# Kernel optimization log

Hardware: AMD Instinct MI355X
Metric: run time of the kernel (lower is better)

The kernel has to match this reference:

```python
import jax, jax.numpy as jnp
import numpy as np
import math

N_HEADS = 16
D_MODEL = 1024
DK = D_MODEL // N_HEADS
B, S = 2, 2048


def setup_inputs() -> dict:
    key = jax.random.key(0)
    ks = jax.random.split(key, 11)
    scale_in = 1.0 / math.sqrt(D_MODEL)
    scale_o = 1.0 / math.sqrt(N_HEADS * DK)
    return {
        "query": jax.random.normal(ks[0], (B, S, D_MODEL), jnp.float32),
        "key": jax.random.normal(ks[1], (B, S, D_MODEL), jnp.float32),
        "value": jax.random.normal(ks[2], (B, S, D_MODEL), jnp.float32),
        # stacked per-head projection weights [H, d_model, dk], biases [H, dk]
        "Wq": jax.random.normal(ks[3], (N_HEADS, D_MODEL, DK), jnp.float32) * scale_in,
        "bq": jax.random.normal(ks[4], (N_HEADS, DK), jnp.float32) * scale_in,
        "Wk": jax.random.normal(ks[5], (N_HEADS, D_MODEL, DK), jnp.float32) * scale_in,
        "bk": jax.random.normal(ks[6], (N_HEADS, DK), jnp.float32) * scale_in,
        "Wv": jax.random.normal(ks[7], (N_HEADS, D_MODEL, DK), jnp.float32) * scale_in,
        "bv": jax.random.normal(ks[8], (N_HEADS, DK), jnp.float32) * scale_in,
        "Wo": jax.random.normal(ks[9], (N_HEADS * DK, D_MODEL), jnp.float32) * scale_o,
        "bo": jax.random.normal(ks[10], (D_MODEL,), jnp.float32) * scale_o,
    }


def reference(query, key, value, Wq, bq, Wk, bk, Wv, bv, Wo, bo):
    # Per-head linear projections, vectorized over heads: [B,H,S,dk]
    q = jnp.einsum("bsd,hdk->bhsk", query, Wq) + bq[None, :, None, :]
    k = jnp.einsum("bsd,hdk->bhsk", key, Wk) + bk[None, :, None, :]
    v = jnp.einsum("bsd,hdk->bhsk", value, Wv) + bv[None, :, None, :]
    # Scaled dot-product scores [B,H,S,S]
    scores = jnp.einsum("bhsk,bhtk->bhst", q, k) / jnp.sqrt(jnp.asarray(DK, q.dtype))
    # FAITHFUL to source: nn.Softmax(dim=0) -> softmax over the BATCH axis
    attn = jax.nn.softmax(scores, axis=0)
    out = jnp.einsum("bhst,bhtk->bhsk", attn, v)  # [B,H,S,dk]
    # concat heads along feature dim (torch.cat dim=2)
    concat = out.transpose(0, 2, 1, 3).reshape(query.shape[0], query.shape[1], N_HEADS * DK)
    return concat @ Wo + bo
```

## Files before the change

kernel.cpp:

```cpp
#include <hip/hip_runtime.h>
#include <hip/hip_bf16.h>

#define B_ 2
#define S_ 2048
#define D_ 1024
#define H_ 16
#define DK_ 64
#define BS_ (B_ * S_)

typedef unsigned int u32;
typedef unsigned short u16;
typedef __attribute__((ext_vector_type(8))) short bf16x8;
typedef __attribute__((ext_vector_type(4))) float f32x4;

__device__ __forceinline__ float bf2f(u16 v) {
    union { u32 u; float f; } c; c.u = ((u32)v) << 16; return c.f;
}
__device__ __forceinline__ u16 f2bf(float f) {
    union { float f; u32 u; } c; c.f = f;
    u32 u = c.u;
    return (u16)((u + 0x7fffu + ((u >> 16) & 1u)) >> 16);
}
__device__ __forceinline__ u32 packtr(float lo, float hi) {
    union { float f; u32 u; } a, b; a.f = lo; b.f = hi;
    return __builtin_amdgcn_perm(b.u, a.u, 0x07060302u);
}
__device__ __forceinline__ int sw64(int r, int c8) { return (((c8) + (r)) & 7) * 8; }

struct WArgs { const float* W[4]; u16* WT[4]; float* csums; };
__global__ __launch_bounds__(256) void prep_w(WArgs wa)
{
    __shared__ __attribute__((aligned(16))) u16 T[64][72];
    const int z = blockIdx.z;
    const float* W = wa.W[z];
    u16* WT = wa.WT[z];
    const int headMode = (z < 3) ? 1 : 0;
    const int tid = threadIdx.x;
    if (z == 0 && blockIdx.x == 0 && blockIdx.y == 0) {
        float4 zz = {0.f, 0.f, 0.f, 0.f};
        *(float4*)(wa.csums + tid * 4) = zz;
    }
    const int k0 = blockIdx.x * 64;
    const int n0 = blockIdx.y * 64;
    const int kr = tid >> 4;
    const int n4 = (tid & 15) * 4;
    #pragma unroll
    for (int pass = 0; pass < 4; ++pass) {
        int kk = k0 + pass * 16 + kr;
        const float* p = headMode
            ? (W + (size_t)((n0 + n4) >> 6) * (1024 * 64) + kk * 64 + ((n0 + n4) & 63))
            : (W + (size_t)kk * 1024 + n0 + n4);
        float4 a = *(const float4*)p;
        int krel = pass * 16 + kr;
        T[n4 + 0][krel] = f2bf(a.x);
        T[n4 + 1][krel] = f2bf(a.y);
        T[n4 + 2][krel] = f2bf(a.z);
        T[n4 + 3][krel] = f2bf(a.w);
    }
    __syncthreads();
    const int nr = tid >> 2;
    const int kq = (tid & 3) * 16;
    uint4 o0 = *(const uint4*)&T[nr][kq];
    uint4 o1 = *(const uint4*)&T[nr][kq + 8];
    u16* q = WT + (size_t)(n0 + nr) * 1024 + k0 + kq;
    *(uint4*)q = o0;
    *(uint4*)(q + 8) = o1;
}

__global__ __launch_bounds__(256) void vprep(
    const u16* __restrict__ Vb, u16* __restrict__ VT, float* __restrict__ csums)
{
    __shared__ __attribute__((aligned(16))) u16 T[64][72];
    __shared__ float red[256];
    const int tid = threadIdx.x;
    const int t0 = blockIdx.x * 64;
    const int bh = blockIdx.y;
    const int b = bh >> 4, h = bh & 15;
    const int tr = tid >> 4;
    const int d4 = (tid & 15) * 4;
    #pragma unroll
    for (int pass = 0; pass < 4; ++pass) {
        int tt = t0 + pass * 16 + tr;
        const u16* p = Vb + (size_t)(b * S_ + tt) * 1024 + h * 64 + d4;
        u32 a = *(const u32*)p;
        u32 c = *(const u32*)(p + 2);
        int trel = pass * 16 + tr;
        T[d4 + 0][trel] = (u16)a;
        T[d4 + 1][trel] = (u16)(a >> 16);
        T[d4 + 2][trel] = (u16)c;
        T[d4 + 3][trel] = (u16)(c >> 16);
    }
    __syncthreads();
    const int dr = tid >> 2;
    const int tq = (tid & 3) * 16;
    uint4 o0 = *(const uint4*)&T[dr][tq];
    uint4 o1 = *(const uint4*)&T[dr][tq + 8];
    u16* q = VT + ((size_t)bh * 64 + dr) * 2048 + t0 + tq;
    *(uint4*)q = o0;
    *(uint4*)(q + 8) = o1;

    if (b == 1) {
        const int dk = tid & 63, part = tid >> 6;
        float s = 0.f;
        #pragma unroll
        for (int t = 0; t < 16; ++t) s += bf2f(T[dk][part * 16 + t]);
        red[tid] = s;
        __syncthreads();
        if (tid < 64)
            atomicAdd(&csums[h * 64 + tid],
                      red[tid] + red[tid + 64] + red[tid + 128] + red[tid + 192]);
    }
}

struct ProjArgs {
    const float* X[3];
    const u16* W[3];
    const float* bias[3];
    u16* Y[3];
};
__global__ __launch_bounds__(256) void proj3(ProjArgs pa)
{
    __shared__ __attribute__((aligned(16))) u16 As[128][72];
    __shared__ __attribute__((aligned(16))) u16 Bs[128][72];
    const int z = blockIdx.z;
    const float* X = pa.X[z];
    const u16* WT = pa.W[z];
    const float* bias = pa.bias[z];
    u16* Y = pa.Y[z];
    const int neg = (z == 1);

    const int tid = threadIdx.x;
    const int lane = tid & 63;
    const int wave = tid >> 6;
    const int quad = lane >> 4;
    const int l16 = lane & 15;
    const int m0 = blockIdx.x * 128;
    const int n0 = blockIdx.y * 128;
    const int wm = (wave & 1) * 64, wn = (wave >> 1) * 64;

    const int srow = tid >> 1;
    const int scol = (tid & 1) * 32;

    f32x4 acc[4][4] = {};

    for (int k0 = 0; k0 < 1024; k0 += 64) {
        __syncthreads();
        {
            const float* p = X + (size_t)(m0 + srow) * 1024 + k0 + scol;
            #pragma unroll
            for (int j = 0; j < 2; ++j) {
                float4 a0 = *(const float4*)(p + j * 16 + 0);
                float4 a1 = *(const float4*)(p + j * 16 + 4);
                float4 a2 = *(const float4*)(p + j * 16 + 8);
                float4 a3 = *(const float4*)(p + j * 16 + 12);
                uint4 w0 = make_uint4(packtr(a0.x, a0.y), packtr(a0.z, a0.w),
                                      packtr(a1.x, a1.y), packtr(a1.z, a1.w));
                uint4 w1 = make_uint4(packtr(a2.x, a2.y), packtr(a2.z, a2.w),
                                      packtr(a3.x, a3.y), packtr(a3.z, a3.w));
                *(uint4*)&As[srow][scol + j * 16]     = w0;
                *(uint4*)&As[srow][scol + j * 16 + 8] = w1;
            }
            const u16* q = WT + (size_t)(n0 + srow) * 1024 + k0 + scol;
            #pragma unroll
            for (int j = 0; j < 4; ++j)
                *(uint4*)&Bs[srow][scol + j * 8] = *(const uint4*)(q + j * 8);
        }
        __syncthreads();
        #pragma unroll
        for (int ks = 0; ks < 2; ++ks) {
            bf16x8 af[4], bfr[4];
            #pragma unroll
            for (int mt = 0; mt < 4; ++mt)
                af[mt] = *(const bf16x8*)&As[wm + mt * 16 + l16][ks * 32 + quad * 8];
            #pragma unroll
            for (int nt = 0; nt < 4; ++nt)
                bfr[nt] = *(const bf16x8*)&Bs[wn + nt * 16 + l16][ks * 32 + quad * 8];
            #pragma unroll
            for (int mt = 0; mt < 4; ++mt)
                #pragma unroll
                for (int nt = 0; nt < 4; ++nt)
                    acc[mt][nt] = __builtin_amdgcn_mfma_f32_16x16x32_bf16(
                        af[mt], bfr[nt], acc[mt][nt], 0, 0, 0);
        }
    }

    #pragma unroll
    for (int nt = 0; nt < 4; ++nt) {
        const int col = n0 + wn + nt * 16 + l16;
        const float bv = bias[col];
        #pragma unroll
        for (int mt = 0; mt < 4; ++mt) {
            #pragma unroll
            for (int r = 0; r < 4; ++r) {
                const int row = m0 + wm + mt * 16 + quad * 4 + r;
                float v = acc[mt][nt][r] + bv;
                if (neg && row >= 2048) v = -v;
                Y[(size_t)row * 1024 + col] = f2bf(v);
            }
        }
    }
}

__global__ __launch_bounds__(256) void gemm_out(
    const u16* __restrict__ X, const u16* __restrict__ WT,
    const float* __restrict__ bias, float* __restrict__ Y)
{
    __shared__ __attribute__((aligned(16))) u16 As[128][72];
    __shared__ __attribute__((aligned(16))) u16 Bs[64][72];
    const int tid = threadIdx.x;
    const int lane = tid & 63;
    const int wave = tid >> 6;
    const int quad = lane >> 4;
    const int l16 = lane & 15;
    const int m0 = blockIdx.x * 128;
    const int n0 = blockIdx.y * 64;
    const int wm = (wave & 1) * 64, wn = (wave >> 1) * 32;

    const int srow = tid >> 1;
    const int scol = (tid & 1) * 32;
    const int brow = tid >> 2;
    const int bcol = (tid & 3) * 16;

    f32x4 acc[4][2] = {};

    for (int k0 = 0; k0 < 1024; k0 += 64) {
        __syncthreads();
        {
            const u16* p = X + (size_t)(m0 + srow) * 1024 + k0 + scol;
            #pragma unroll
            for (int j = 0; j < 4; ++j)
                *(uint4*)&As[srow][scol + j * 8] = *(const uint4*)(p + j * 8);
            const u16* q = WT + (size_t)(n0 + brow) * 1024 + k0 + bcol;
            *(uint4*)&Bs[brow][bcol]     = *(const uint4*)q;
            *(uint4*)&Bs[brow][bcol + 8] = *(const uint4*)(q + 8);
        }
        __syncthreads();
        #pragma unroll
        for (int ks = 0; ks < 2; ++ks) {
            bf16x8 af[4], bfr[2];
            #pragma unroll
            for (int mt = 0; mt < 4; ++mt)
                af[mt] = *(const bf16x8*)&As[wm + mt * 16 + l16][ks * 32 + quad * 8];
            #pragma unroll
            for (int nt = 0; nt < 2; ++nt)
                bfr[nt] = *(const bf16x8*)&Bs[wn + nt * 16 + l16][ks * 32 + quad * 8];
            #pragma unroll
            for (int mt = 0; mt < 4; ++mt)
                #pragma unroll
                for (int nt = 0; nt < 2; ++nt)
                    acc[mt][nt] = __builtin_amdgcn_mfma_f32_16x16x32_bf16(
                        af[mt], bfr[nt], acc[mt][nt], 0, 0, 0);
        }
    }

    #pragma unroll
    for (int nt = 0; nt < 2; ++nt) {
        const int col = n0 + wn + nt * 16 + l16;
        const float bv = bias[col];
        #pragma unroll
        for (int mt = 0; mt < 4; ++mt) {
            #pragma unroll
            for (int r = 0; r < 4; ++r) {
                const int row = m0 + wm + mt * 16 + quad * 4 + r;
                Y[(size_t)row * 1024 + col] = acc[mt][nt][r] + bv;
            }
        }
    }
}

__global__ __launch_bounds__(256) void attn_mfma(
    const u16* __restrict__ Qb, const u16* __restrict__ Kb,
    const u16* __restrict__ VT, const float* __restrict__ csums,
    u16* __restrict__ Cc)
{
    __shared__ __attribute__((aligned(16))) u16 Ks[2][64][64];
    __shared__ __attribute__((aligned(16))) u16 Vs[2][64][64];
    __shared__ __attribute__((aligned(16))) u16 Ps[64][64];

    const int id = blockIdx.x;
    const int xcd = id & 7, j = id >> 3;
    const int h = xcd + 8 * (j >> 5);
    const int s0 = (j & 31) * 64;

    const int tid = threadIdx.x;
    const int lane = tid & 63;
    const int wave = tid >> 6;
    const int quad = lane >> 4;
    const int l16 = lane & 15;
    const int sw = wave * 16;

    const int r_ = tid >> 2;
    const int cq = (tid & 3) * 16;
    const int cq8 = (tid & 3) * 2;

    bf16x8 qf[2][2];
    #pragma unroll
    for (int b = 0; b < 2; ++b)
        #pragma unroll
        for (int ks = 0; ks < 2; ++ks)
            qf[b][ks] = *(const bf16x8*)(Qb + (size_t)(b * S_ + s0 + sw + l16) * 1024
                                          + h * 64 + ks * 32 + quad * 8);

    f32x4 O0[4] = {}, T1[4] = {};

    for (int t0 = 0; t0 < S_; t0 += 64) {
        __syncthreads();
        #pragma unroll
        for (int b = 0; b < 2; ++b) {
            const u16* pk = Kb + (size_t)(b * S_ + t0 + r_) * 1024 + h * 64 + cq;
            *(uint4*)&Ks[b][r_][sw64(r_, cq8)]     = *(const uint4*)pk;
            *(uint4*)&Ks[b][r_][sw64(r_, cq8 + 1)] = *(const uint4*)(pk + 8);
            const u16* pv = VT + ((size_t)(b * H_ + h) * 64 + r_) * 2048 + t0 + cq;
            *(uint4*)&Vs[b][r_][sw64(r_, cq8)]     = *(const uint4*)pv;
            *(uint4*)&Vs[b][r_][sw64(r_, cq8 + 1)] = *(const uint4*)(pv + 8);
        }
        __syncthreads();

        f32x4 dacc[4] = {};
        #pragma unroll
        for (int mt = 0; mt < 4; ++mt) {
            const int kr = mt * 16 + l16;
            #pragma unroll
            for (int ks = 0; ks < 2; ++ks) {
                bf16x8 k0f = *(const bf16x8*)&Ks[0][kr][sw64(kr, ks * 4 + quad)];
                dacc[mt] = __builtin_amdgcn_mfma_f32_16x16x32_bf16(k0f, qf[0][ks], dacc[mt], 0, 0, 0);
                bf16x8 k1f = *(const bf16x8*)&Ks[1][kr][sw64(kr, ks * 4 + quad)];
                dacc[mt] = __builtin_amdgcn_mfma_f32_16x16x32_bf16(k1f, qf[1][ks], dacc[mt], 0, 0, 0);
            }
        }
        const int pr = sw + l16;
        #pragma unroll
        for (int mt = 0; mt < 4; ++mt) {
            float p[4];
            #pragma unroll
            for (int r = 0; r < 4; ++r) {
                float e = __expf(dacc[mt][r] * -0.125f);
                p[r] = __builtin_amdgcn_rcpf(1.0f + e);
            }
            uint2 w;
            w.x = packtr(p[0], p[1]);
            w.y = packtr(p[2], p[3]);
            const int c8 = 2 * mt + (quad >> 1);
            *(uint2*)&Ps[pr][sw64(pr, c8) + (quad & 1) * 4] = w;
        }
        bf16x8 pf0 = *(const bf16x8*)&Ps[pr][sw64(pr, quad)];
        bf16x8 pf1 = *(const bf16x8*)&Ps[pr][sw64(pr, 4 + quad)];
        #pragma unroll
        for (int nt = 0; nt < 4; ++nt) {
            const int vr = nt * 16 + l16;
            bf16x8 v00 = *(const bf16x8*)&Vs[0][vr][sw64(vr, quad)];
            bf16x8 v01 = *(const bf16x8*)&Vs[0][vr][sw64(vr, 4 + quad)];
            O0[nt] = __builtin_amdgcn_mfma_f32_16x16x32_bf16(pf0, v00, O0[nt], 0, 0, 0);
            O0[nt] = __builtin_amdgcn_mfma_f32_16x16x32_bf16(pf1, v01, O0[nt], 0, 0, 0);
            bf16x8 v10 = *(const bf16x8*)&Vs[1][vr][sw64(vr, quad)];
            bf16x8 v11 = *(const bf16x8*)&Vs[1][vr][sw64(vr, 4 + quad)];
            T1[nt] = __builtin_amdgcn_mfma_f32_16x16x32_bf16(pf0, v10, T1[nt], 0, 0, 0);
            T1[nt] = __builtin_amdgcn_mfma_f32_16x16x32_bf16(pf1, v11, T1[nt], 0, 0, 0);
        }
    }

    #pragma unroll
    for (int nt = 0; nt < 4; ++nt) {
        const int dk = nt * 16 + l16;
        const float cs1 = csums[h * 64 + dk];
        #pragma unroll
        for (int r = 0; r < 4; ++r) {
            const int s = s0 + sw + quad * 4 + r;
            Cc[(size_t)(0 * S_ + s) * 1024 + h * 64 + dk] = f2bf(O0[nt][r]);
            Cc[(size_t)(1 * S_ + s) * 1024 + h * 64 + dk] = f2bf(cs1 - T1[nt][r]);
        }
    }
}

extern "C" void kernel_launch(void* const* d_in, const int* in_sizes, int n_in,
                              void* d_out, int out_size, void* d_ws, size_t ws_size,
                              hipStream_t stream) {
    const float* q  = (const float*)d_in[0];
    const float* k  = (const float*)d_in[1];
    const float* v  = (const float*)d_in[2];
    const float* Wq = (const float*)d_in[3];
    const float* bq = (const float*)d_in[4];
    const float* Wk = (const float*)d_in[5];
    const float* bk = (const float*)d_in[6];
    const float* Wv = (const float*)d_in[7];
    const float* bv = (const float*)d_in[8];
    const float* Wo = (const float*)d_in[9];
    const float* bo = (const float*)d_in[10];

    char* ws = (char*)d_ws;
    const size_t MB = 1024 * 1024;
    u16* Cc  = (u16*)(ws);
    u16* WqT = (u16*)(ws + 8  * MB);
    u16* WkT = (u16*)(ws + 10 * MB);
    u16* WvT = (u16*)(ws + 12 * MB);
    u16* WoT = (u16*)(ws + 14 * MB);
    u16* Qp  = (u16*)(ws + 16 * MB);
    u16* Kp  = (u16*)(ws + 24 * MB);
    u16* Vp  = (u16*)(ws + 32 * MB);
    u16* VTv = (u16*)(ws + 40 * MB);
    float* csums = (float*)d_out;

    dim3 blk(256);

    WArgs wa;
    wa.W[0] = Wq; wa.W[1] = Wk; wa.W[2] = Wv; wa.W[3] = Wo;
    wa.WT[0] = WqT; wa.WT[1] = WkT; wa.WT[2] = WvT; wa.WT[3] = WoT;
    wa.csums = csums;
    prep_w<<<dim3(16, 16, 4), blk, 0, stream>>>(wa);

    ProjArgs pa;
    pa.X[0] = q;  pa.X[1] = k;  pa.X[2] = v;
    pa.W[0] = WqT; pa.W[1] = WkT; pa.W[2] = WvT;
    pa.bias[0] = bq; pa.bias[1] = bk; pa.bias[2] = bv;
    pa.Y[0] = Qp; pa.Y[1] = Kp; pa.Y[2] = Vp;
    proj3<<<dim3(32, 8, 3), blk, 0, stream>>>(pa);

    vprep<<<dim3(32, 32), blk, 0, stream>>>(Vp, VTv, csums);
    attn_mfma<<<dim3(512), blk, 0, stream>>>(Qp, Kp, VTv, csums, Cc);
    gemm_out<<<dim3(32, 16), blk, 0, stream>>>(Cc, WoT, bo, (float*)d_out);
}
```

Baseline: 259.2 us.

## Pre-convert inputs to bf16 and use direct global-to-LDS async loads in GEMMs

```diff
diff --git a/kernel.cpp b/kernel.cpp
--- a/kernel.cpp
+++ b/kernel.cpp
@@ -13,6 +13,13 @@
 typedef __attribute__((ext_vector_type(8))) short bf16x8;
 typedef __attribute__((ext_vector_type(4))) float f32x4;
 
+typedef const __attribute__((address_space(1))) void glb_cv;
+typedef __attribute__((address_space(3))) void lds_v;
+
+__device__ __forceinline__ void async_cp16(const void* g, void* l) {
+    __builtin_amdgcn_global_load_lds((glb_cv*)g, (lds_v*)l, 16, 0, 0);
+}
+
 __device__ __forceinline__ float bf2f(u16 v) {
     union { u32 u; float f; } c; c.u = ((u32)v) << 16; return c.f;
 }
@@ -21,27 +28,49 @@
     u32 u = c.u;
     return (u16)((u + 0x7fffu + ((u >> 16) & 1u)) >> 16);
 }
+__device__ __forceinline__ u32 pack2(float a, float b) {
+    return (u32)f2bf(a) | ((u32)f2bf(b) << 16);
+}
 __device__ __forceinline__ u32 packtr(float lo, float hi) {
     union { float f; u32 u; } a, b; a.f = lo; b.f = hi;
     return __builtin_amdgcn_perm(b.u, a.u, 0x07060302u);
 }
 __device__ __forceinline__ int sw64(int r, int c8) { return (((c8) + (r)) & 7) * 8; }
 
-struct WArgs { const float* W[4]; u16* WT[4]; float* csums; };
-__global__ __launch_bounds__(256) void prep_w(WArgs wa)
+struct PrepArgs {
+    const float* W[4]; u16* WT[4];
+    const float* X[3]; u16* XB[3];
+    float* csums;
+};
+__global__ __launch_bounds__(256) void prep(PrepArgs a)
 {
+    const int id = blockIdx.x;
+    const int tid = threadIdx.x;
+    if (id >= 1024) {
+        const int cid = id - 1024;
+        const int z = cid >> 11;
+        const size_t base = (size_t)(cid & 2047) * 2048 + tid * 8;
+        const float* X = a.X[z];
+        float4 x0 = *(const float4*)(X + base);
+        float4 x1 = *(const float4*)(X + base + 4);
+        uint4 o;
+        o.x = pack2(x0.x, x0.y); o.y = pack2(x0.z, x0.w);
+        o.z = pack2(x1.x, x1.y); o.w = pack2(x1.z, x1.w);
+        *(uint4*)(a.XB[z] + base) = o;
+        return;
+    }
+    if (id == 0) {
+        float4 zz = {0.f, 0.f, 0.f, 0.f};
+        *(float4*)(a.csums + tid * 4) = zz;
+    }
     __shared__ __attribute__((aligned(16))) u16 T[64][72];
-    const int z = blockIdx.z;
-    const float* W = wa.W[z];
-    u16* WT = wa.WT[z];
+    const int z = id >> 8;
+    const int rem = id & 255;
+    const float* W = a.W[z];
+    u16* WT = a.WT[z];
     const int headMode = (z < 3) ? 1 : 0;
-    const int tid = threadIdx.x;
-    if (z == 0 && blockIdx.x == 0 && blockIdx.y == 0) {
-        float4 zz = {0.f, 0.f, 0.f, 0.f};
-        *(float4*)(wa.csums + tid * 4) = zz;
-    }
-    const int k0 = blockIdx.x * 64;
-    const int n0 = blockIdx.y * 64;
+    const int k0 = (rem >> 4) * 64;
+    const int n0 = (rem & 15) * 64;
     const int kr = tid >> 4;
     const int n4 = (tid & 15) * 4;
     #pragma unroll
@@ -50,12 +79,12 @@
         const float* p = headMode
             ? (W + (size_t)((n0 + n4) >> 6) * (1024 * 64) + kk * 64 + ((n0 + n4) & 63))
             : (W + (size_t)kk * 1024 + n0 + n4);
-        float4 a = *(const float4*)p;
+        float4 v = *(const float4*)p;
         int krel = pass * 16 + kr;
-        T[n4 + 0][krel] = f2bf(a.x);
-        T[n4 + 1][krel] = f2bf(a.y);
-        T[n4 + 2][krel] = f2bf(a.z);
-        T[n4 + 3][krel] = f2bf(a.w);
+        T[n4 + 0][krel] = f2bf(v.x);
+        T[n4 + 1][krel] = f2bf(v.y);
+        T[n4 + 2][krel] = f2bf(v.z);
+        T[n4 + 3][krel] = f2bf(v.w);
     }
     __syncthreads();
     const int nr = tid >> 2;
@@ -113,17 +142,17 @@
 }
 
 struct ProjArgs {
-    const float* X[3];
+    const u16* X[3];
     const u16* W[3];
     const float* bias[3];
     u16* Y[3];
 };
 __global__ __launch_bounds__(256) void proj3(ProjArgs pa)
 {
-    __shared__ __attribute__((aligned(16))) u16 As[128][72];
-    __shared__ __attribute__((aligned(16))) u16 Bs[128][72];
+    __shared__ __attribute__((aligned(16))) u16 As[128][32];
+    __shared__ __attribute__((aligned(16))) u16 Bs[128][32];
     const int z = blockIdx.z;
-    const float* X = pa.X[z];
+    const u16* X = pa.X[z];
     const u16* WT = pa.W[z];
     const float* bias = pa.bias[z];
     u16* Y = pa.Y[z];
@@ -138,50 +167,34 @@
     const int n0 = blockIdx.y * 128;
     const int wm = (wave & 1) * 64, wn = (wave >> 1) * 64;
 
-    const int srow = tid >> 1;
-    const int scol = (tid & 1) * 32;
-
     f32x4 acc[4][4] = {};
 
-    for (int k0 = 0; k0 < 1024; k0 += 64) {
-        __syncthreads();
-        {
-            const float* p = X + (size_t)(m0 + srow) * 1024 + k0 + scol;
-            #pragma unroll
-            for (int j = 0; j < 2; ++j) {
-                float4 a0 = *(const float4*)(p + j * 16 + 0);
-                float4 a1 = *(const float4*)(p + j * 16 + 4);
-                float4 a2 = *(const float4*)(p + j * 16 + 8);
-                float4 a3 = *(const float4*)(p + j * 16 + 12);
-                uint4 w0 = make_uint4(packtr(a0.x, a0.y), packtr(a0.z, a0.w),
-                                      packtr(a1.x, a1.y), packtr(a1.z, a1.w));
-                uint4 w1 = make_uint4(packtr(a2.x, a2.y), packtr(a2.z, a2.w),
-                                      packtr(a3.x, a3.y), packtr(a3.z, a3.w));
-                *(uint4*)&As[srow][scol + j * 16]     = w0;
-                *(uint4*)&As[srow][scol + j * 16 + 8] = w1;
-            }
-            const u16* q = WT + (size_t)(n0 + srow) * 1024 + k0 + scol;
-            #pragma unroll
-            for (int j = 0; j < 4; ++j)
-                *(uint4*)&Bs[srow][scol + j * 8] = *(const uint4*)(q + j * 8);
-        }
-        __syncthreads();
-        #pragma unroll
-        for (int ks = 0; ks < 2; ++ks) {
-            bf16x8 af[4], bfr[4];
-            #pragma unroll
-            for (int mt = 0; mt < 4; ++mt)
-                af[mt] = *(const bf16x8*)&As[wm + mt * 16 + l16][ks * 32 + quad * 8];
+    for (int k0 = 0; k0 < 1024; k0 += 32) {
+        __syncthreads();
+        #pragma unroll
+        for (int call = 0; call < 2; ++call) {
+            const int c = tid + call * 256;
+            const int row = c >> 2, cc = (c & 3) * 8;
+            char* la = (char*)&As[0][0] + (size_t)(c & ~63) * 16;
+            async_cp16(X + (size_t)(m0 + row) * 1024 + k0 + cc, la);
+            char* lb = (char*)&Bs[0][0] + (size_t)(c & ~63) * 16;
+            async_cp16(WT + (size_t)(n0 + row) * 1024 + k0 + cc, lb);
+        }
+        __syncthreads();
+
+        bf16x8 af[4], bfr[4];
+        #pragma unroll
+        for (int mt = 0; mt < 4; ++mt)
+            af[mt] = *(const bf16x8*)&As[wm + mt * 16 + l16][quad * 8];
+        #pragma unroll
+        for (int nt = 0; nt < 4; ++nt)
+            bfr[nt] = *(const bf16x8*)&Bs[wn + nt * 16 + l16][quad * 8];
+        #pragma unroll
+        for (int mt = 0; mt < 4; ++mt)
             #pragma unroll
             for (int nt = 0; nt < 4; ++nt)
-                bfr[nt] = *(const bf16x8*)&Bs[wn + nt * 16 + l16][ks * 32 + quad * 8];
-            #pragma unroll
-            for (int mt = 0; mt < 4; ++mt)
-                #pragma unroll
-                for (int nt = 0; nt < 4; ++nt)
-                    acc[mt][nt] = __builtin_amdgcn_mfma_f32_16x16x32_bf16(
-                        af[mt], bfr[nt], acc[mt][nt], 0, 0, 0);
-        }
+                acc[mt][nt] = __builtin_amdgcn_mfma_f32_16x16x32_bf16(
+                    af[mt], bfr[nt], acc[mt][nt], 0, 0, 0);
     }
 
     #pragma unroll
@@ -205,8 +218,8 @@
     const u16* __restrict__ X, const u16* __restrict__ WT,
     const float* __restrict__ bias, float* __restrict__ Y)
 {
-    __shared__ __attribute__((aligned(16))) u16 As[128][72];
-    __shared__ __attribute__((aligned(16))) u16 Bs[64][72];
+    __shared__ __attribute__((aligned(16))) u16 As[128][32];
+    __shared__ __attribute__((aligned(16))) u16 Bs[64][32];
     const int tid = threadIdx.x;
     const int lane = tid & 63;
     const int wave = tid >> 6;
@@ -216,41 +229,38 @@
     const int n0 = blockIdx.y * 64;
     const int wm = (wave & 1) * 64, wn = (wave >> 1) * 32;
 
-    const int srow = tid >> 1;
-    const int scol = (tid & 1) * 32;
-    const int brow = tid >> 2;
-    const int bcol = (tid & 3) * 16;
-
     f32x4 acc[4][2] = {};
 
-    for (int k0 = 0; k0 < 1024; k0 += 64) {
-        __syncthreads();
+    for (int k0 = 0; k0 < 1024; k0 += 32) {
+        __syncthreads();
+        #pragma unroll
+        for (int call = 0; call < 2; ++call) {
+            const int c = tid + call * 256;
+            const int row = c >> 2, cc = (c & 3) * 8;
+            char* la = (char*)&As[0][0] + (size_t)(c & ~63) * 16;
+            async_cp16(X + (size_t)(m0 + row) * 1024 + k0 + cc, la);
+        }
         {
-            const u16* p = X + (size_t)(m0 + srow) * 1024 + k0 + scol;
-            #pragma unroll
-            for (int j = 0; j < 4; ++j)
-                *(uint4*)&As[srow][scol + j * 8] = *(const uint4*)(p + j * 8);
-            const u16* q = WT + (size_t)(n0 + brow) * 1024 + k0 + bcol;
-            *(uint4*)&Bs[brow][bcol]     = *(const uint4*)q;
-            *(uint4*)&Bs[brow][bcol + 8] = *(const uint4*)(q + 8);
-        }
-        __syncthreads();
-        #pragma unroll
-        for (int ks = 0; ks < 2; ++ks) {
-            bf16x8 af[4], bfr[2];
-            #pragma unroll
-            for (int mt = 0; mt < 4; ++mt)
-                af[mt] = *(const bf16x8*)&As[wm + mt * 16 + l16][ks * 32 + quad * 8];
+            const int c = tid;
+            const int row = c >> 2, cc = (c & 3) * 8;
+            char* lb = (char*)&Bs[0][0] + (size_t)(c & ~63) * 16;
+            async_cp16(WT + (size_t)(n0 + row) * 1024 + k0 + cc, lb);
+        }
+        __syncthreads();
+
+        bf16x8 af[4], bfr[2];
+        #pragma unroll
+        for (int mt = 0; mt < 4; ++mt)
+            af[mt] = *(const bf16x8*)&As[wm + mt * 16 + l16][quad * 8];
+        #pragma unroll
+        for (int nt = 0; nt < 2; ++nt)
+            bfr[nt] = *(const bf16x8*)&Bs[wn + nt * 16 + l16][quad * 8];
+        #pragma unroll
+        for (int mt = 0; mt < 4; ++mt)
             #pragma unroll
             for (int nt = 0; nt < 2; ++nt)
-                bfr[nt] = *(const bf16x8*)&Bs[wn + nt * 16 + l16][ks * 32 + quad * 8];
-            #pragma unroll
-            for (int mt = 0; mt < 4; ++mt)
-                #pragma unroll
-                for (int nt = 0; nt < 2; ++nt)
-                    acc[mt][nt] = __builtin_amdgcn_mfma_f32_16x16x32_bf16(
-                        af[mt], bfr[nt], acc[mt][nt], 0, 0, 0);
-        }
+                acc[mt][nt] = __builtin_amdgcn_mfma_f32_16x16x32_bf16(
+                    af[mt], bfr[nt], acc[mt][nt], 0, 0, 0);
     }
 
     #pragma unroll
@@ -390,6 +400,7 @@
     char* ws = (char*)d_ws;
     const size_t MB = 1024 * 1024;
     u16* Cc  = (u16*)(ws);
+    u16* Xq  = (u16*)(ws);
     u16* WqT = (u16*)(ws + 8  * MB);
     u16* WkT = (u16*)(ws + 10 * MB);
     u16* WvT = (u16*)(ws + 12 * MB);
@@ -398,18 +409,22 @@
     u16* Kp  = (u16*)(ws + 24 * MB);
     u16* Vp  = (u16*)(ws + 32 * MB);
     u16* VTv = (u16*)(ws + 40 * MB);
+    u16* Xk  = (u16*)(ws + 40 * MB);
+    u16* Xv  = (u16*)(ws + 48 * MB);
     float* csums = (float*)d_out;
 
     dim3 blk(256);
 
-    WArgs wa;
-    wa.W[0] = Wq; wa.W[1] = Wk; wa.W[2] = Wv; wa.W[3] = Wo;
-    wa.WT[0] = WqT; wa.WT[1] = WkT; wa.WT[2] = WvT; wa.WT[3] = WoT;
-    wa.csums = csums;
-    prep_w<<<dim3(16, 16, 4), blk, 0, stream>>>(wa);
+    PrepArgs pr;
+    pr.W[0] = Wq; pr.W[1] = Wk; pr.W[2] = Wv; pr.W[3] = Wo;
+    pr.WT[0] = WqT; pr.WT[1] = WkT; pr.WT[2] = WvT; pr.WT[3] = WoT;
+    pr.X[0] = q; pr.X[1] = k; pr.X[2] = v;
+    pr.XB[0] = Xq; pr.XB[1] = Xk; pr.XB[2] = Xv;
+    pr.csums = csums;
+    prep<<<dim3(1024 + 6144), blk, 0, stream>>>(pr);
 
     ProjArgs pa;
-    pa.X[0] = q;  pa.X[1] = k;  pa.X[2] = v;
+    pa.X[0] = Xq; pa.X[1] = Xk; pa.X[2] = Xv;
     pa.W[0] = WqT; pa.W[1] = WkT; pa.W[2] = WvT;
     pa.bias[0] = bq; pa.bias[1] = bk; pa.bias[2] = bv;
     pa.Y[0] = Qp; pa.Y[1] = Kp; pa.Y[2] = Vp;
```

New measurement: 239.7 us. 7.5% less time.
